# Optimization experiments

Hardware: AMD Instinct MI355X
Metric: run time of the kernel (lower is better)

## Reference

```python
import jax, jax.numpy as jnp
import numpy as np
import math

B, C, MAPS, HEADS, F, W = 2, 8, 4, 8, 256, 1024
HD = F // HEADS  # head dim = 32


def conv2d(x, w, b):
    # x [B,Ci,H,W], w [Co,Ci,3,3], SAME padding 1
    y = jax.lax.conv_general_dilated(x, w, (1, 1), [(1, 1), (1, 1)],
                                     dimension_numbers=('NCHW', 'OIHW', 'NCHW'))
    return y + b[None, :, None, None]


def mcl_feat(x, w):
    # MultichannelLinear feature transform: per-channel linear over feature dim
    # x [B,C,Fin,W], w [C,Fout,Fin] -> [B,C,Fout,W]
    return jnp.einsum('bcfw,cgf->bcgw', x, w)


def rope(x):
    # lucidrains-style rotary embedding over seq dim (-2); x [..., S, D]
    d = x.shape[-1]
    s = x.shape[-2]
    inv = 1.0 / (10000.0 ** (jnp.arange(0, d, 2, dtype=jnp.float32) / d))
    fr = jnp.arange(s, dtype=jnp.float32)[:, None] * inv[None, :]  # [S, D/2]
    cos = jnp.repeat(jnp.cos(fr), 2, axis=-1).astype(x.dtype)  # [S, D]
    sin = jnp.repeat(jnp.sin(fr), 2, axis=-1).astype(x.dtype)
    x2 = x.reshape(*x.shape[:-1], d // 2, 2)
    xr = jnp.stack((-x2[..., 1], x2[..., 0]), axis=-1).reshape(x.shape)
    return x * cos + xr * sin


def setup_inputs() -> dict:
    key = jax.random.key(0)
    ks = jax.random.split(key, 16)
    p = lambda k, shp, s=0.02: (jax.random.normal(k, shp, dtype=jnp.float32) * s)
    inp = {
        'x': jax.random.normal(ks[0], (B, C, F, W), dtype=jnp.float32),
        'prev_qk': jax.random.normal(ks[1], (B, MAPS, HEADS, W, W), dtype=jnp.float32),
        'wq_conv': p(ks[2], (MAPS, C, 3, 3)), 'bq_conv': jnp.zeros((MAPS,), jnp.float32),
        'wq_lin': p(ks[3], (MAPS, F, F)),
        'wk_conv': p(ks[4], (MAPS, C, 3, 3)), 'bk_conv': jnp.zeros((MAPS,), jnp.float32),
        'wk_lin': p(ks[5], (MAPS, F, F)),
        'wv_conv': p(ks[6], (MAPS, C, 3, 3)), 'bv_conv': jnp.zeros((MAPS,), jnp.float32),
        'wv_lin': p(ks[7], (MAPS, F, F)),
        'wo_pw': p(ks[8], (C + MAPS, F, F)),
        'wo_dw': p(ks[9], (C, C + MAPS)),
    }
    return inp


def reference(x, prev_qk, wq_conv, bq_conv, wq_lin, wk_conv, bk_conv, wk_lin,
              wv_conv, bv_conv, wv_lin, wo_pw, wo_dw):
    b, c, h, w = x.shape

    def proj(w_conv, b_conv, w_lin):
        y = mcl_feat(conv2d(x, w_conv, b_conv), w_lin)  # [B,M,F,W]
        # transpose(2,3) -> [B,M,W,F] -> split heads -> [B,M,Hd,W? ] permute
        y = y.transpose(0, 1, 3, 2).reshape(b, MAPS, w, HEADS, HD)
        return y.transpose(0, 1, 3, 2, 4)  # [B,M,Heads,W,HD]

    q = rope(proj(wq_conv, bq_conv, wq_lin))
    k = rope(proj(wk_conv, bk_conv, wk_lin))
    v = proj(wv_conv, bv_conv, wv_lin)

    # NOTE: scale is sqrt(h) = sqrt(feature/height dim), as in the original code
    qk = jnp.einsum('bmnqd,bmnkd->bmnqk', q, k) / math.sqrt(h)
    qk = qk + prev_qk
    a = jnp.einsum('bmnqk,bmnkd->bmnqd', jax.nn.softmax(qk, axis=-1), v)
    # [B,M,Heads,W,HD] -> [B,M,W,Heads*HD] -> [B,M,F,W]
    a = a.transpose(0, 1, 3, 2, 4).reshape(b, MAPS, w, -1).transpose(0, 1, 3, 2)

    cat = jnp.concatenate((x, a), axis=1)  # [B, C+M, F, W]
    out = jnp.einsum('bcfw,oc->bofw', mcl_feat(cat, wo_pw), wo_dw)  # o_proj
    return out, qk
```

## Files before the change

### kernel.cpp

```cpp
#include <hip/hip_runtime.h>
#include <hip/hip_bf16.h>
#include <stdint.h>


typedef __attribute__((ext_vector_type(8))) short s16x8;
typedef __attribute__((ext_vector_type(4))) float f32x4;

#define MFMA16(a, b, c) __builtin_amdgcn_mfma_f32_16x16x32_bf16((a), (b), (c), 0, 0, 0)

__device__ __forceinline__ short f2bf(float f) {
  unsigned u = __builtin_bit_cast(unsigned, f);
  u = (u + 0x7FFFu + ((u >> 16) & 1u)) >> 16;
  return (short)u;
}
__device__ __forceinline__ unsigned pack2(float a, float b) {
  return (unsigned)(unsigned short)f2bf(a) | ((unsigned)(unsigned short)f2bf(b) << 16);
}
__device__ __forceinline__ float bf2f(unsigned u) {
  return __builtin_bit_cast(float, u << 16);
}

__global__ __launch_bounds__(256) void k_prep(const float* wq, const float* wk,
                                              const float* wv, const float* wo,
                                              short* wlin, short* wob, float* ct, float* st) {
  int i = blockIdx.x * 256 + threadIdx.x;
  if (i < 262144) wlin[i] = f2bf(wq[i]);
  else if (i < 524288) wlin[i] = f2bf(wk[i - 262144]);
  else if (i < 786432) wlin[i] = f2bf(wv[i - 524288]);
  if (i < 786432) wob[i] = f2bf(wo[i]);
  if (i < 16384) {
    int w = i >> 4, j = i & 15;
    float inv = exp2f(-(float)j * (13.287712379549449f / 16.0f));
    float ang = (float)w * inv;
    ct[i] = cosf(ang);
    st[i] = sinf(ang);
  }
}

__device__ __forceinline__ void loadrow(float* r, const float* xc, int f, int w0) {
  if (f < 0 || f > 255) {
#pragma unroll
    for (int jj = 0; jj < 6; ++jj) r[jj] = 0.f;
    return;
  }
  const float* row = xc + f * 1024;
#pragma unroll
  for (int jj = 0; jj < 6; ++jj) {
    int wc = w0 - 1 + jj;
    r[jj] = (wc >= 0 && wc < 1024) ? row[wc] : 0.f;
  }
}

__global__ __launch_bounds__(256) void k_conv(const float* x, const float* wqc, const float* bq,
                                              const float* wkc, const float* bk,
                                              const float* wvc, const float* bv, short* y) {
  int blk = blockIdx.x;
  int m_ = blk >> 7;
  int b_ = (blk >> 6) & 1;
  int fs = blk & 63;
  int f0 = fs * 4;
  int w0 = threadIdx.x * 4;
  const float* xb = x + (size_t)b_ * 2097152;
  const float* wp_[3] = {wqc + m_ * 72, wkc + m_ * 72, wvc + m_ * 72};
  float bias_[3] = {bq[m_], bk[m_], bv[m_]};

  float acc[3][4][4];
#pragma unroll
  for (int p = 0; p < 3; ++p)
#pragma unroll
    for (int fi = 0; fi < 4; ++fi)
#pragma unroll
      for (int j = 0; j < 4; ++j) acc[p][fi][j] = bias_[p];

  for (int c = 0; c < 8; ++c) {
    const float* xc = xb + c * 262144;
    float w9[3][9];
#pragma unroll
    for (int p = 0; p < 3; ++p)
#pragma unroll
      for (int t = 0; t < 9; ++t) w9[p][t] = wp_[p][c * 9 + t];
    float rows[6][6];
#pragma unroll
    for (int ri = 0; ri < 6; ++ri) loadrow(rows[ri], xc, f0 - 1 + ri, w0);
#pragma unroll
    for (int fi = 0; fi < 4; ++fi) {
#pragma unroll
      for (int p = 0; p < 3; ++p) {
#pragma unroll
        for (int j = 0; j < 4; ++j) {
          float s = acc[p][fi][j];
          s += rows[fi][j] * w9[p][0] + rows[fi][j + 1] * w9[p][1] + rows[fi][j + 2] * w9[p][2];
          s += rows[fi + 1][j] * w9[p][3] + rows[fi + 1][j + 1] * w9[p][4] + rows[fi + 1][j + 2] * w9[p][5];
          s += rows[fi + 2][j] * w9[p][6] + rows[fi + 2][j + 1] * w9[p][7] + rows[fi + 2][j + 2] * w9[p][8];
          acc[p][fi][j] = s;
        }
      }
    }
  }
#pragma unroll
  for (int p = 0; p < 3; ++p) {
    int mat = p * 8 + b_ * 4 + m_;
    short* yp = y + (size_t)mat * 262144;
#pragma unroll
    for (int fi = 0; fi < 4; ++fi) {
      uint2 pk;
      pk.x = pack2(acc[p][fi][0], acc[p][fi][1]);
      pk.y = pack2(acc[p][fi][2], acc[p][fi][3]);
      *(uint2*)(yp + (f0 + fi) * 1024 + w0) = pk;
    }
  }
}

__global__ __launch_bounds__(256) void k_qkv(const short* wlin, const short* y,
                                             const float* ct, const float* st,
                                             short* qws, short* kws, short* vws) {
  __shared__ short ytile[64][264];
  int blk = blockIdx.x;
  int pbm = blk >> 4, wt = blk & 15;
  int p = pbm >> 3, bm = pbm & 7;
  int m_ = bm & 3;
  int tid = threadIdx.x, wv = tid >> 6, l = tid & 63, lr = l & 15, lg = l >> 4;
  const short* wl = wlin + (p * 4 + m_) * 65536;
  const short* yp = y + (size_t)pbm * 262144;
  int w0 = wt * 64;
  int G0 = wv * 64;

  {
    int h2 = l >> 5, lih = l & 31;
#pragma unroll
    for (int i = 0; i < 32; ++i) {
      int f = wv * 64 + i * 2 + h2;
      unsigned u = *(const unsigned*)(yp + f * 1024 + w0 + lih * 2);
      ytile[lih * 2][f] = (short)(u & 0xffffu);
      ytile[lih * 2 + 1][f] = (short)(u >> 16);
    }
  }
  __syncthreads();

  f32x4 acc[4][4];
#pragma unroll
  for (int i = 0; i < 4; ++i)
#pragma unroll
    for (int j = 0; j < 4; ++j) acc[i][j] = (f32x4){0.f, 0.f, 0.f, 0.f};

  if (p < 2) {
    for (int kc = 0; kc < 256; kc += 32) {
      s16x8 A[4], Bf[4];
#pragma unroll
      for (int gs = 0; gs < 4; ++gs)
        A[gs] = *(const s16x8*)(wl + (G0 + gs * 16 + lr) * 256 + kc + lg * 8);
#pragma unroll
      for (int s = 0; s < 4; ++s)
        Bf[s] = *(const s16x8*)(&ytile[s * 16 + lr][kc + lg * 8]);
#pragma unroll
      for (int gs = 0; gs < 4; ++gs)
#pragma unroll
        for (int s = 0; s < 4; ++s) acc[gs][s] = MFMA16(A[gs], Bf[s], acc[gs][s]);
    }
    short* dst = (p == 0) ? qws : kws;
    float scale = (p == 0) ? 0.0625f : 1.0f;
#pragma unroll
    for (int gs = 0; gs < 4; ++gs) {
      int g0v = G0 + gs * 16 + lg * 4;
      int h = g0v >> 5, d0 = g0v & 31;
      int i0 = d0 >> 1;
#pragma unroll
      for (int s = 0; s < 4; ++s) {
        int w = w0 + s * 16 + lr;
        float c0 = ct[w * 16 + i0], sn0 = st[w * 16 + i0];
        float c1 = ct[w * 16 + i0 + 1], sn1 = st[w * 16 + i0 + 1];
        f32x4 v = acc[gs][s];
        float e0 = (v[0] * c0 - v[1] * sn0) * scale;
        float e1 = (v[1] * c0 + v[0] * sn0) * scale;
        float e2 = (v[2] * c1 - v[3] * sn1) * scale;
        float e3 = (v[3] * c1 + v[2] * sn1) * scale;
        uint2 pk;
        pk.x = pack2(e0, e1);
        pk.y = pack2(e2, e3);
        *(uint2*)(dst + (((size_t)bm * 8 + h) * 1024 + w) * 32 + d0) = pk;
      }
    }
  } else {
    for (int kc = 0; kc < 256; kc += 32) {
      s16x8 A[4], Bf[4];
#pragma unroll
      for (int s = 0; s < 4; ++s)
        A[s] = *(const s16x8*)(&ytile[s * 16 + lr][kc + lg * 8]);
#pragma unroll
      for (int gs = 0; gs < 4; ++gs)
        Bf[gs] = *(const s16x8*)(wl + (G0 + gs * 16 + lr) * 256 + kc + lg * 8);
#pragma unroll
      for (int s = 0; s < 4; ++s)
#pragma unroll
        for (int gs = 0; gs < 4; ++gs) acc[s][gs] = MFMA16(A[s], Bf[gs], acc[s][gs]);
    }
#pragma unroll
    for (int s = 0; s < 4; ++s) {
      int wb = w0 + s * 16 + lg * 4;
#pragma unroll
      for (int gs = 0; gs < 4; ++gs) {
        int g = G0 + gs * 16 + lr;
        f32x4 v = acc[s][gs];
        uint2 pk;
        pk.x = pack2(v[0], v[1]);
        pk.y = pack2(v[2], v[3]);
        *(uint2*)(vws + ((size_t)bm * 256 + g) * 1024 + wb) = pk;
      }
    }
  }
}

__global__ __launch_bounds__(256, 1) void k_attn(const short* qws, const short* kws,
                                                 const short* vws, const float* prev,
                                                 float* qko, short* aT) {
  __shared__ char smem[155648];
  int blk = blockIdx.x;
  int bmh = blk >> 4;
  int qg = blk & 15;
  int h = bmh & 7, bm = bmh >> 3;
  int tid = threadIdx.x;
  int wv = tid >> 6, l = tid & 63, lr = l & 15, lg = l >> 4;
  const short* kp = kws + (size_t)bmh * 32768;
  const short* vp = vws + ((size_t)bm * 256 + h * 32) * 1024;

  {
    int row4 = tid >> 2, c = tid & 3;
#pragma unroll
    for (int i = 0; i < 16; ++i) {
      int row = i * 64 + row4;
      s16x8 kv = *(const s16x8*)(kp + row * 32 + c * 8);
      *(s16x8*)(smem + row * 64 + ((c * 16) ^ ((row & 3) << 4))) = kv;
    }
    int g2 = tid >> 7, cb = (tid & 127) * 16;
#pragma unroll
    for (int i = 0; i < 16; ++i) {
      int g = i * 2 + g2;
      s16x8 vv = *(const s16x8*)(vp + g * 1024 + (cb >> 1));
      *(s16x8*)(smem + 65536 + g * 2048 + (cb ^ ((g & 7) << 4))) = vv;
    }
  }
  __syncthreads();

  int q0 = qg * 64 + wv * 16;
  const short* qp = qws + (size_t)bmh * 32768;
  s16x8 qf = *(const s16x8*)(qp + (q0 + lr) * 32 + lg * 8);
  char* Sb = smem + 131072 + wv * 4096;
  char* Pb = smem + 147456 + wv * 2048;
  const float* pvb = prev + (size_t)bmh * 1048576 + (size_t)q0 * 1024;
  float* qob = qko + (size_t)bmh * 1048576 + (size_t)q0 * 1024;
  int pcol = (l & 15) * 4;
  int pcolb = pcol * 4;
  f32x4 o0 = {0.f, 0.f, 0.f, 0.f}, o1 = {0.f, 0.f, 0.f, 0.f};
  f32x4 rs = {0.f, 0.f, 0.f, 0.f};
  const f32x4 z4 = {0.f, 0.f, 0.f, 0.f};

  auto attn_win = [&](int w, f32x4(&pr)[4]) {
    int k0 = w * 64;
#pragma unroll
    for (int s = 0; s < 4; ++s) {
      int krow = k0 + s * 16 + lr;
      s16x8 kf = *(const s16x8*)(smem + krow * 64 + ((lg * 16) ^ ((krow & 3) << 4)));
      f32x4 sx = MFMA16(kf, qf, z4);
      *(f32x4*)(Sb + lr * 256 + ((s * 64 + lg * 16) ^ ((lr & 7) << 4))) = sx;
    }
#pragma unroll
    for (int j = 0; j < 4; ++j) {
      int qr = j * 4 + lg;
      f32x4 sv = *(const f32x4*)(Sb + qr * 256 + (pcolb ^ ((qr & 7) << 4)));
      f32x4 v = sv + pr[j];
      *(f32x4*)(qob + (size_t)qr * 1024 + k0 + pcol) = v;
      float e0 = __expf(v[0]), e1 = __expf(v[1]);
      float e2 = __expf(v[2]), e3 = __expf(v[3]);
      rs[j] += (e0 + e1) + (e2 + e3);
      uint2 pk;
      pk.x = pack2(e0, e1);
      pk.y = pack2(e2, e3);
      *(uint2*)(Pb + qr * 128 + (((l & 15) * 8) ^ ((qr & 7) << 4))) = pk;
    }
    if (w + 2 < 16) {
#pragma unroll
      for (int j = 0; j < 4; ++j)
        pr[j] = *(const f32x4*)(pvb + (size_t)(j * 4 + lg) * 1024 + (w + 2) * 64 + pcol);
    }
#pragma unroll
    for (int kc = 0; kc < 2; ++kc) {
      s16x8 pa = *(const s16x8*)(Pb + lr * 128 + ((kc * 64 + lg * 16) ^ ((lr & 7) << 4)));
      int kcb = (k0 + kc * 32 + lg * 8) * 2;
      s16x8 vf0 = *(const s16x8*)(smem + 65536 + lr * 2048 + (kcb ^ ((lr & 7) << 4)));
      o0 = MFMA16(pa, vf0, o0);
      s16x8 vf1 = *(const s16x8*)(smem + 65536 + (16 + lr) * 2048 + (kcb ^ ((lr & 7) << 4)));
      o1 = MFMA16(pa, vf1, o1);
    }
  };

  f32x4 pA[4], pB[4];
#pragma unroll
  for (int j = 0; j < 4; ++j)
    pA[j] = *(const f32x4*)(pvb + (size_t)(j * 4 + lg) * 1024 + 0 + pcol);
#pragma unroll
  for (int j = 0; j < 4; ++j)
    pB[j] = *(const f32x4*)(pvb + (size_t)(j * 4 + lg) * 1024 + 64 + pcol);

  for (int w = 0; w < 16; w += 2) {
    attn_win(w, pA);
    attn_win(w + 1, pB);
  }

#pragma unroll
  for (int j = 0; j < 4; ++j) {
    float s = rs[j];
    s += __shfl_xor(s, 1);
    s += __shfl_xor(s, 2);
    s += __shfl_xor(s, 4);
    s += __shfl_xor(s, 8);
    rs[j] = s;
  }
  if (lr == 0) {
#pragma unroll
    for (int j = 0; j < 4; ++j) *(float*)(Sb + (j * 4 + lg) * 4) = rs[j];
  }
  f32x4 sums = *(const f32x4*)(Sb + lg * 16);
  f32x4 inv = {1.f / sums[0], 1.f / sums[1], 1.f / sums[2], 1.f / sums[3]};
  o0 *= inv;
  o1 *= inv;
  short* ap = aT + (size_t)bm * 262144;
#pragma unroll
  for (int r = 0; r < 4; ++r) {
    int row = q0 + lg * 4 + r;
    ap[row * 256 + h * 32 + lr] = f2bf(o0[r]);
    ap[row * 256 + h * 32 + 16 + lr] = f2bf(o1[r]);
  }
}

__global__ __launch_bounds__(256) void k_zproj(const short* wopw, const float* x,
                                               const short* aT, short* z) {
  __shared__ short xtile[64][264];
  int blk = blockIdx.x;
  int bc = blk >> 4, wt = blk & 15;
  int b_ = bc / 12, c_ = bc % 12;
  const short* wl = wopw + c_ * 65536;
  int tid = threadIdx.x, wv = tid >> 6, l = tid & 63, lr = l & 15, lg = l >> 4;
  int w0 = wt * 64, G0 = wv * 64;
  bool use_lds = (c_ < 8);
  const short* asrc = aT + ((size_t)b_ * 4 + (c_ - 8)) * 262144;

  if (use_lds) {
    const float* xp = x + ((size_t)b_ * 8 + c_) * 262144;
    int h2 = l >> 5, lih = l & 31;
#pragma unroll
    for (int i = 0; i < 32; ++i) {
      int f = wv * 64 + i * 2 + h2;
      uint2 u = *(const uint2*)(xp + f * 1024 + w0 + lih * 2);
      xtile[lih * 2][f] = f2bf(__builtin_bit_cast(float, u.x));
      xtile[lih * 2 + 1][f] = f2bf(__builtin_bit_cast(float, u.y));
    }
  }
  __syncthreads();

  f32x4 acc[4][4];
#pragma unroll
  for (int i = 0; i < 4; ++i)
#pragma unroll
    for (int j = 0; j < 4; ++j) acc[i][j] = (f32x4){0.f, 0.f, 0.f, 0.f};
  for (int kc = 0; kc < 256; kc += 32) {
    s16x8 A[4], Bf[4];
#pragma unroll
    for (int s = 0; s < 4; ++s)
      A[s] = use_lds ? *(const s16x8*)(&xtile[s * 16 + lr][kc + lg * 8])
                     : *(const s16x8*)(asrc + (w0 + s * 16 + lr) * 256 + kc + lg * 8);
#pragma unroll
    for (int gs = 0; gs < 4; ++gs)
      Bf[gs] = *(const s16x8*)(wl + (G0 + gs * 16 + lr) * 256 + kc + lg * 8);
#pragma unroll
    for (int s = 0; s < 4; ++s)
#pragma unroll
      for (int gs = 0; gs < 4; ++gs) acc[s][gs] = MFMA16(A[s], Bf[gs], acc[s][gs]);
  }
  short* zp = z + (size_t)bc * 262144;
#pragma unroll
  for (int s = 0; s < 4; ++s) {
    int wb = w0 + s * 16 + lg * 4;
#pragma unroll
    for (int gs = 0; gs < 4; ++gs) {
      int g = G0 + gs * 16 + lr;
      f32x4 v = acc[s][gs];
      uint2 pk;
      pk.x = pack2(v[0], v[1]);
      pk.y = pack2(v[2], v[3]);
      *(uint2*)(zp + g * 1024 + wb) = pk;
    }
  }
}

__global__ __launch_bounds__(256) void k_dw(const short* z, const float* dw, float* out0) {
  __shared__ float wdw[96];
  if (threadIdx.x < 96) wdw[threadIdx.x] = dw[threadIdx.x];
  __syncthreads();
  int id = blockIdx.x * 256 + threadIdx.x;
  int w4 = id & 255, g = (id >> 8) & 255, b_ = id >> 16;
  const short* zb = z + ((size_t)b_ * 12) * 262144 + g * 1024 + w4 * 4;
  float zv[12][4];
#pragma unroll
  for (int c = 0; c < 12; ++c) {
    uint2 u = *(const uint2*)(zb + (size_t)c * 262144);
    zv[c][0] = bf2f(u.x & 0xffffu);
    zv[c][1] = bf2f(u.x >> 16);
    zv[c][2] = bf2f(u.y & 0xffffu);
    zv[c][3] = bf2f(u.y >> 16);
  }
  float* ob = out0 + ((size_t)b_ * 8) * 262144 + g * 1024 + w4 * 4;
#pragma unroll
  for (int o = 0; o < 8; ++o) {
    f32x4 s = {0.f, 0.f, 0.f, 0.f};
#pragma unroll
    for (int c = 0; c < 12; ++c) {
      float wc = wdw[o * 12 + c];
      s[0] += wc * zv[c][0];
      s[1] += wc * zv[c][1];
      s[2] += wc * zv[c][2];
      s[3] += wc * zv[c][3];
    }
    *(f32x4*)(ob + (size_t)o * 262144) = s;
  }
}

extern "C" void kernel_launch(void* const* d_in, const int* in_sizes, int n_in,
                              void* d_out, int out_size, void* d_ws, size_t ws_size,
                              hipStream_t stream) {
  const float* x = (const float*)d_in[0];
  const float* prevqk = (const float*)d_in[1];
  const float* wq_conv = (const float*)d_in[2];
  const float* bq = (const float*)d_in[3];
  const float* wq_lin = (const float*)d_in[4];
  const float* wk_conv = (const float*)d_in[5];
  const float* bk = (const float*)d_in[6];
  const float* wk_lin = (const float*)d_in[7];
  const float* wv_conv = (const float*)d_in[8];
  const float* bv = (const float*)d_in[9];
  const float* wv_lin = (const float*)d_in[10];
  const float* wo_pw = (const float*)d_in[11];
  const float* wo_dw = (const float*)d_in[12];

  float* out0 = (float*)d_out;
  float* qkout = out0 + 4194304;

  char* ws = (char*)d_ws;
  short* wlin_b = (short*)ws;
  short* wopw_b = wlin_b + 786432;
  float* ct = (float*)(ws + 3145728);
  float* st = ct + 16384;
  short* y_b = (short*)(ws + 3276800);
  short* q_b = y_b + 6291456;
  short* k_b = q_b + 2097152;
  short* v_b = k_b + 2097152;
  short* aT_b = v_b + 2097152;
  short* z_b = (short*)(ws + 53608448);

  k_prep<<<3072, 256, 0, stream>>>(wq_lin, wk_lin, wv_lin, wo_pw, wlin_b, wopw_b, ct, st);
  k_conv<<<512, 256, 0, stream>>>(x, wq_conv, bq, wk_conv, bk, wv_conv, bv, y_b);
  k_qkv<<<384, 256, 0, stream>>>(wlin_b, y_b, ct, st, q_b, k_b, v_b);
  k_attn<<<1024, 256, 0, stream>>>(q_b, k_b, v_b, prevqk, qkout, aT_b);
  k_zproj<<<384, 256, 0, stream>>>(wopw_b, x, aT_b, z_b);
  k_dw<<<512, 256, 0, stream>>>(z_b, wo_dw, out0);
}
```

Baseline: 220.6 us.

## Fuse pointwise output projection with depthwise mix and deepen prev_qk prefetch

Merges k_zproj and k_dw into one k_out kernel. Each block computes the per-channel feature GEMM for all 12 input channels of a 32x64 output tile and immediately accumulates the 8 depthwise outputs in registers, so the bf16 z intermediate is never written to or read from global memory. The attention kernel also prefetches prev_qk four windows ahead instead of two, using four register buffers. Costs: only 256 blocks with less MFMA work per wave, extra __syncthreads per channel, 64 accumulator registers per thread, and higher register pressure in attention.

```diff
diff --git a/kernel.cpp b/kernel.cpp
--- a/kernel.cpp
+++ b/kernel.cpp
@@ -277,10 +277,10 @@
       pk.y = pack2(e2, e3);
       *(uint2*)(Pb + qr * 128 + (((l & 15) * 8) ^ ((qr & 7) << 4))) = pk;
     }
-    if (w + 2 < 16) {
+    if (w + 4 < 16) {
 #pragma unroll
       for (int j = 0; j < 4; ++j)
-        pr[j] = *(const f32x4*)(pvb + (size_t)(j * 4 + lg) * 1024 + (w + 2) * 64 + pcol);
+        pr[j] = *(const f32x4*)(pvb + (size_t)(j * 4 + lg) * 1024 + (w + 4) * 64 + pcol);
     }
 #pragma unroll
     for (int kc = 0; kc < 2; ++kc) {
@@ -293,17 +293,25 @@
     }
   };
 
-  f32x4 pA[4], pB[4];
+  f32x4 pA[4], pB[4], pC[4], pD[4];
 #pragma unroll
   for (int j = 0; j < 4; ++j)
     pA[j] = *(const f32x4*)(pvb + (size_t)(j * 4 + lg) * 1024 + 0 + pcol);
 #pragma unroll
   for (int j = 0; j < 4; ++j)
     pB[j] = *(const f32x4*)(pvb + (size_t)(j * 4 + lg) * 1024 + 64 + pcol);
-
-  for (int w = 0; w < 16; w += 2) {
+#pragma unroll
+  for (int j = 0; j < 4; ++j)
+    pC[j] = *(const f32x4*)(pvb + (size_t)(j * 4 + lg) * 1024 + 128 + pcol);
+#pragma unroll
+  for (int j = 0; j < 4; ++j)
+    pD[j] = *(const f32x4*)(pvb + (size_t)(j * 4 + lg) * 1024 + 192 + pcol);
+
+  for (int w = 0; w < 16; w += 4) {
     attn_win(w, pA);
     attn_win(w + 1, pB);
+    attn_win(w + 2, pC);
+    attn_win(w + 3, pD);
   }
 
 #pragma unroll
@@ -332,96 +340,67 @@
   }
 }
 
-__global__ __launch_bounds__(256) void k_zproj(const short* wopw, const float* x,
-                                               const short* aT, short* z) {
+__global__ __launch_bounds__(256) void k_out(const short* wopw, const float* x,
+                                             const short* aT, const float* dw, float* out0) {
   __shared__ short xtile[64][264];
+  __shared__ float wdw[96];
   int blk = blockIdx.x;
-  int bc = blk >> 4, wt = blk & 15;
-  int b_ = bc / 12, c_ = bc % 12;
-  const short* wl = wopw + c_ * 65536;
+  int b_ = blk >> 7;
+  int gt = (blk >> 4) & 7;
+  int wt = blk & 15;
+  int g0 = gt * 32, w0 = wt * 64;
   int tid = threadIdx.x, wv = tid >> 6, l = tid & 63, lr = l & 15, lg = l >> 4;
-  int w0 = wt * 64, G0 = wv * 64;
-  bool use_lds = (c_ < 8);
-  const short* asrc = aT + ((size_t)b_ * 4 + (c_ - 8)) * 262144;
-
-  if (use_lds) {
-    const float* xp = x + ((size_t)b_ * 8 + c_) * 262144;
-    int h2 = l >> 5, lih = l & 31;
-#pragma unroll
-    for (int i = 0; i < 32; ++i) {
-      int f = wv * 64 + i * 2 + h2;
-      uint2 u = *(const uint2*)(xp + f * 1024 + w0 + lih * 2);
-      xtile[lih * 2][f] = f2bf(__builtin_bit_cast(float, u.x));
-      xtile[lih * 2 + 1][f] = f2bf(__builtin_bit_cast(float, u.y));
-    }
-  }
-  __syncthreads();
-
-  f32x4 acc[4][4];
-#pragma unroll
-  for (int i = 0; i < 4; ++i)
-#pragma unroll
-    for (int j = 0; j < 4; ++j) acc[i][j] = (f32x4){0.f, 0.f, 0.f, 0.f};
-  for (int kc = 0; kc < 256; kc += 32) {
-    s16x8 A[4], Bf[4];
-#pragma unroll
-    for (int s = 0; s < 4; ++s)
-      A[s] = use_lds ? *(const s16x8*)(&xtile[s * 16 + lr][kc + lg * 8])
-                     : *(const s16x8*)(asrc + (w0 + s * 16 + lr) * 256 + kc + lg * 8);
-#pragma unroll
-    for (int gs = 0; gs < 4; ++gs)
-      Bf[gs] = *(const s16x8*)(wl + (G0 + gs * 16 + lr) * 256 + kc + lg * 8);
-#pragma unroll
-    for (int s = 0; s < 4; ++s)
-#pragma unroll
-      for (int gs = 0; gs < 4; ++gs) acc[s][gs] = MFMA16(A[s], Bf[gs], acc[s][gs]);
-  }
-  short* zp = z + (size_t)bc * 262144;
-#pragma unroll
-  for (int s = 0; s < 4; ++s) {
-    int wb = w0 + s * 16 + lg * 4;
-#pragma unroll
-    for (int gs = 0; gs < 4; ++gs) {
-      int g = G0 + gs * 16 + lr;
-      f32x4 v = acc[s][gs];
-      uint2 pk;
-      pk.x = pack2(v[0], v[1]);
-      pk.y = pack2(v[2], v[3]);
-      *(uint2*)(zp + g * 1024 + wb) = pk;
-    }
-  }
-}
-
-__global__ __launch_bounds__(256) void k_dw(const short* z, const float* dw, float* out0) {
-  __shared__ float wdw[96];
-  if (threadIdx.x < 96) wdw[threadIdx.x] = dw[threadIdx.x];
-  __syncthreads();
-  int id = blockIdx.x * 256 + threadIdx.x;
-  int w4 = id & 255, g = (id >> 8) & 255, b_ = id >> 16;
-  const short* zb = z + ((size_t)b_ * 12) * 262144 + g * 1024 + w4 * 4;
-  float zv[12][4];
-#pragma unroll
+  if (tid < 96) wdw[tid] = dw[tid];
+
+  f32x4 oacc[8][2];
+#pragma unroll
+  for (int o = 0; o < 8; ++o)
+#pragma unroll
+    for (int gs = 0; gs < 2; ++gs) oacc[o][gs] = (f32x4){0.f, 0.f, 0.f, 0.f};
+  const f32x4 z4 = {0.f, 0.f, 0.f, 0.f};
+
   for (int c = 0; c < 12; ++c) {
-    uint2 u = *(const uint2*)(zb + (size_t)c * 262144);
-    zv[c][0] = bf2f(u.x & 0xffffu);
-    zv[c][1] = bf2f(u.x >> 16);
-    zv[c][2] = bf2f(u.y & 0xffffu);
-    zv[c][3] = bf2f(u.y >> 16);
-  }
-  float* ob = out0 + ((size_t)b_ * 8) * 262144 + g * 1024 + w4 * 4;
-#pragma unroll
-  for (int o = 0; o < 8; ++o) {
-    f32x4 s = {0.f, 0.f, 0.f, 0.f};
-#pragma unroll
-    for (int c = 0; c < 12; ++c) {
+    const short* wl = wopw + c * 65536;
+    bool use_lds = (c < 8);
+    const short* asrc = aT + ((size_t)b_ * 4 + (c - 8)) * 262144;
+    if (use_lds) {
+      __syncthreads();
+      const float* xp = x + ((size_t)b_ * 8 + c) * 262144;
+      int h2 = l >> 5, lih = l & 31;
+#pragma unroll
+      for (int i = 0; i < 32; ++i) {
+        int f = wv * 64 + i * 2 + h2;
+        uint2 u = *(const uint2*)(xp + f * 1024 + w0 + lih * 2);
+        xtile[lih * 2][f] = f2bf(__builtin_bit_cast(float, u.x));
+        xtile[lih * 2 + 1][f] = f2bf(__builtin_bit_cast(float, u.y));
+      }
+      __syncthreads();
+    }
+    f32x4 zacc0 = z4, zacc1 = z4;
+    for (int kc = 0; kc < 256; kc += 32) {
+      s16x8 A = use_lds ? *(const s16x8*)(&xtile[wv * 16 + lr][kc + lg * 8])
+                        : *(const s16x8*)(asrc + (w0 + wv * 16 + lr) * 256 + kc + lg * 8);
+      s16x8 B0 = *(const s16x8*)(wl + (g0 + lr) * 256 + kc + lg * 8);
+      s16x8 B1 = *(const s16x8*)(wl + (g0 + 16 + lr) * 256 + kc + lg * 8);
+      zacc0 = MFMA16(A, B0, zacc0);
+      zacc1 = MFMA16(A, B1, zacc1);
+    }
+#pragma unroll
+    for (int o = 0; o < 8; ++o) {
       float wc = wdw[o * 12 + c];
-      s[0] += wc * zv[c][0];
-      s[1] += wc * zv[c][1];
-      s[2] += wc * zv[c][2];
-      s[3] += wc * zv[c][3];
-    }
-    *(f32x4*)(ob + (size_t)o * 262144) = s;
-  }
+      oacc[o][0] += zacc0 * wc;
+      oacc[o][1] += zacc1 * wc;
+    }
+  }
+  float* ob = out0 + (size_t)b_ * 8 * 262144;
+  int wb = w0 + wv * 16 + lg * 4;
+#pragma unroll
+  for (int o = 0; o < 8; ++o)
+#pragma unroll
+    for (int gs = 0; gs < 2; ++gs) {
+      int g = g0 + gs * 16 + lr;
+      *(f32x4*)(ob + (size_t)o * 262144 + g * 1024 + wb) = oacc[o][gs];
+    }
 }
 
 extern "C" void kernel_launch(void* const* d_in, const int* in_sizes, int n_in,
@@ -454,12 +433,10 @@
   short* k_b = q_b + 2097152;
   short* v_b = k_b + 2097152;
   short* aT_b = v_b + 2097152;
-  short* z_b = (short*)(ws + 53608448);
 
   k_prep<<<3072, 256, 0, stream>>>(wq_lin, wk_lin, wv_lin, wo_pw, wlin_b, wopw_b, ct, st);
   k_conv<<<512, 256, 0, stream>>>(x, wq_conv, bq, wk_conv, bk, wv_conv, bv, y_b);
   k_qkv<<<384, 256, 0, stream>>>(wlin_b, y_b, ct, st, q_b, k_b, v_b);
   k_attn<<<1024, 256, 0, stream>>>(q_b, k_b, v_b, prevqk, qkout, aT_b);
-  k_zproj<<<384, 256, 0, stream>>>(wopw_b, x, aT_b, z_b);
-  k_dw<<<512, 256, 0, stream>>>(z_b, wo_dw, out0);
-}
+  k_out<<<256, 256, 0, stream>>>(wopw_b, x, aT_b, wo_dw, out0);
+}
```

After: 328.5 us. 1.49x slower.
